# Optimization experiments

Measured on AMD Instinct MI355X. Metric: run time of the kernel, lower is better.

## Reference

```python
import jax, jax.numpy as jnp
import numpy as np

B, N, K = 4, 4096, 16
C_CONT, C_MOT, HID = 64, 64, 128
FEAT = C_CONT + C_MOT


def _conv2d_1x1(W, b, x):
    # x: [B, Cin, N, K] -> [B, Cout, N, K]
    return jnp.einsum('oc,bcnk->bonk', W, x) + b[None, :, None, None]


def _conv1d_1x1(W, b, x):
    # x: [B, Cin, N] -> [B, Cout, N]
    return jnp.einsum('oc,bcn->bon', W, x) + b[None, :, None]


def setup_inputs() -> dict:
    key = jax.random.key(0)
    ks = jax.random.split(key, 13)
    def w(k, shape):
        fan_in = shape[-1]
        return jax.random.normal(k, shape, dtype=jnp.float32) / np.sqrt(fan_in)
    return {
        'H0': jax.random.normal(ks[0], (B, HID, N), dtype=jnp.float32),
        'points0': jax.random.normal(ks[1], (B, 3, N), dtype=jnp.float32),
        'points1': jax.random.normal(ks[2], (B, 3, N), dtype=jnp.float32),
        'contents1': jax.random.normal(ks[3], (B, C_CONT, N), dtype=jnp.float32),
        'motions1': jax.random.normal(ks[4], (B, C_MOT, N), dtype=jnp.float32),
        'W_R': w(ks[5], (HID, HID + FEAT + 4)),
        'b_R': jnp.zeros((HID,), dtype=jnp.float32),
        'W_Z': w(ks[6], (HID, HID + FEAT + 4)),
        'b_Z': jnp.zeros((HID,), dtype=jnp.float32),
        'W_H0': w(ks[7], (HID, HID + 4)),
        'b_H0': jnp.zeros((HID,), dtype=jnp.float32),
        'W_H1': w(ks[8], (HID, HID + FEAT)),
        'b_H1': jnp.zeros((HID,), dtype=jnp.float32),
    }


def reference(H0, points0, points1, contents1, motions1,
              W_R, b_R, W_Z, b_Z, W_H0, b_H0, W_H1, b_H1):
    p1 = points1.transpose(0, 2, 1)  # [B,N,3] anchors (current frame)
    p0 = points0.transpose(0, 2, 1)  # [B,N,3] queries (last frame)
    # pairwise squared distances [B,N,N]
    sq = (jnp.sum(p1 * p1, -1)[:, :, None]
          + jnp.sum(p0 * p0, -1)[:, None, :]
          - 2.0 * jnp.einsum('bmd,bnd->bmn', p1, p0))
    _, nn_idx = jax.lax.top_k(-sq, K)  # [B,N,K] k-nearest in points0
    # gather neighbor coords and hidden states
    nn_pts = jax.vmap(lambda p, i: p[i])(p0, nn_idx)        # [B,N,K,3]
    nn_H0 = jax.vmap(lambda h, i: h[:, i])(H0, nn_idx)      # [B,C,N,K]
    rela = nn_pts - p1[:, :, None, :]                       # [B,N,K,3]
    dist = jnp.linalg.norm(rela, axis=-1, keepdims=True)    # [B,N,K,1]
    nn_group = jnp.concatenate([rela, dist], -1).transpose(0, 3, 1, 2)  # [B,4,N,K]

    feats = jnp.concatenate([contents1, motions1], axis=1)  # [B,F,N]
    feats_e = jnp.broadcast_to(feats[..., None], feats.shape + (K,))  # [B,F,N,K]

    x_rz = jnp.concatenate([nn_group, nn_H0, feats_e], axis=1)  # [B,4+C+F,N,K]
    gate_R = jax.nn.sigmoid(jnp.max(_conv2d_1x1(W_R, b_R, x_rz), axis=-1))  # [B,C,N]
    gate_Z = jax.nn.sigmoid(jnp.max(_conv2d_1x1(W_Z, b_Z, x_rz), axis=-1))  # [B,C,N]

    x_h = jnp.concatenate([nn_group, nn_H0], axis=1)  # [B,4+C,N,K]
    H1_0 = jnp.max(_conv2d_1x1(W_H0, b_H0, x_h), axis=-1)  # [B,C,N]

    H1_1 = jnp.tanh(_conv1d_1x1(W_H1, b_H1,
                                jnp.concatenate([feats, gate_R * H1_0], axis=1)))
    return gate_Z * H1_0 + (1.0 - gate_Z) * H1_1
```

## Files before the change

### kernel.cpp

```cpp
#include <hip/hip_runtime.h>
#include <math.h>


#define BIGV 1e30f

typedef __attribute__((ext_vector_type(8))) short bf16x8;
typedef __attribute__((ext_vector_type(16))) float f32x16;

#define MFMA32(a, b, c) __builtin_amdgcn_mfma_f32_32x32x16_bf16(a, b, c, 0, 0, 0)

__device__ __forceinline__ unsigned short f2bf(float x) {
  unsigned int u = __float_as_uint(x);
  unsigned int r = u + 0x7fffu + ((u >> 16) & 1u);
  return (unsigned short)(r >> 16);
}

__global__ __launch_bounds__(256) void k_transpose(const float* __restrict__ H0,
                                                   unsigned short* __restrict__ H0tb) {
  __shared__ float tile[16][17];
  int blk = blockIdx.x;
  int b = blk >> 11;
  int rem = blk & 2047;
  int c0 = (rem >> 8) << 4;
  int n0 = (rem & 255) << 4;
  int tr = threadIdx.x >> 4, tc = threadIdx.x & 15;
  tile[tr][tc] = H0[((b << 7) + c0 + tr) * 4096 + n0 + tc];
  __syncthreads();
  H0tb[((b << 12) + n0 + tr) * 128 + c0 + tc] = f2bf(tile[tc][tr]);
}

__global__ __launch_bounds__(256) void k_pack(const float* __restrict__ p0,
                                              float4* __restrict__ P0p) {
  int t = blockIdx.x * 256 + threadIdx.x;
  int b = t >> 12, j = t & 4095;
  const float* P0 = p0 + b * 3 * 4096;
  float x = P0[j], y = P0[4096 + j], z = P0[8192 + j];
  P0p[t] = make_float4(x, y, z, x * x + y * y + z * z);
}

__device__ __forceinline__ unsigned long long knn_key(float v, int j) {
  unsigned int u = __float_as_uint(v);
  unsigned int mask = (unsigned int)(((int)u) >> 31) | 0x80000000u;
  return ((unsigned long long)(u ^ mask) << 32) | (unsigned int)j;
}

__global__ __launch_bounds__(256) void k_knn(const float4* __restrict__ P0p,
                                             const float* __restrict__ p1,
                                             int* __restrict__ nn) {
  const int wv = threadIdx.x >> 6, lane = threadIdx.x & 63;
  const int g = (blockIdx.x << 2) + wv;
  const int b = g >> 12, m = g & 4095;
  const float* P1 = p1 + b * 3 * 4096;
  const float x1 = P1[m], y1 = P1[4096 + m], z1 = P1[8192 + m];
  const float s1 = x1 * x1 + y1 * y1 + z1 * z1;
  const float nx = -2.0f * x1, ny = -2.0f * y1, nz = -2.0f * z1;
  const float4* C = P0p + (b << 12);

  float v0 = BIGV, v1 = BIGV, v2 = BIGV, v3 = BIGV;
  int j0 = 0, j1 = 0, j2 = 0, j3 = 0;
#pragma unroll 8
  for (int t = 0; t < 64; ++t) {
    const int j = (t << 6) + lane;
    float4 c = C[j];
    float sq = fmaf(nz, c.z, fmaf(ny, c.y, fmaf(nx, c.x, s1 + c.w)));
    bool c0_ = sq < v0, c1_ = sq < v1, c2_ = sq < v2, c3_ = sq < v3;
    j3 = c3_ ? (c2_ ? j2 : j) : j3;
    j2 = c2_ ? (c1_ ? j1 : j) : j2;
    j1 = c1_ ? (c0_ ? j0 : j) : j1;
    j0 = c0_ ? j : j0;
    v3 = __builtin_amdgcn_fmed3f(sq, v2, v3);
    v2 = __builtin_amdgcn_fmed3f(sq, v1, v2);
    v1 = __builtin_amdgcn_fmed3f(sq, v0, v1);
    v0 = fminf(sq, v0);
  }

  const unsigned long long INFK = ~0ull;
  unsigned long long k0 = knn_key(v0, j0), k1 = knn_key(v1, j1);
  unsigned long long k2 = knn_key(v2, j2), k3 = knn_key(v3, j3);

  unsigned long long wkey = 0;
  unsigned long long lastk = 0;
#pragma unroll 1
  for (int r = 0; r < 16; ++r) {
    unsigned long long mk;
    if (!__any((int)(k0 == INFK))) {
      mk = k0;
    } else {
      mk = k0;
      if (k0 == INFK) {
#pragma unroll 1
        for (int t = 0; t < 64; ++t) {
          const int j = (t << 6) + lane;
          float4 c = C[j];
          float sq = fmaf(nz, c.z, fmaf(ny, c.y, fmaf(nx, c.x, s1 + c.w)));
          unsigned long long kk = knn_key(sq, j);
          if (kk > lastk && kk < mk) mk = kk;
        }
      }
    }
#pragma unroll
    for (int off = 1; off < 64; off <<= 1) {
      unsigned long long ok = __shfl_xor(mk, off);
      mk = (ok < mk) ? ok : mk;
    }
    if (lane == r) wkey = mk;
    lastk = mk;
    if (k0 == mk) { k0 = k1; k1 = k2; k2 = k3; k3 = INFK; }
  }
  const int ob = ((b << 12) + m) << 4;
  if (lane < 16) nn[ob + lane] = (int)(unsigned int)wkey;
}

__global__ __launch_bounds__(256) void k_prep(const float* __restrict__ W_R,
                                              const float* __restrict__ W_Z,
                                              const float* __restrict__ W_H0,
                                              const float* __restrict__ W_H1,
                                              unsigned short* __restrict__ WmainP,
                                              unsigned short* __restrict__ WfeP) {
  int t = blockIdx.x * 256 + threadIdx.x;
  if (t < 6912) {
    int l = t & 63;
    int f = t >> 6;
    int ks = f % 9, T = f / 9;
    int col = T * 32 + (l & 31);
    int kb = ks * 16 + ((l >> 5) << 3);
    const float* W; int stride, row;
    if (col < 128)      { W = W_R;  stride = 260; row = col; }
    else if (col < 256) { W = W_Z;  stride = 260; row = col - 128; }
    else                { W = W_H0; stride = 132; row = col - 256; }
    unsigned int u[4];
#pragma unroll
    for (int i2 = 0; i2 < 4; ++i2) {
      float a0, a1;
      int k0 = kb + 2 * i2, k1 = k0 + 1;
      a0 = (k0 < 128) ? W[row * stride + 4 + k0] : ((k0 < 132) ? W[row * stride + (k0 - 128)] : 0.f);
      a1 = (k1 < 128) ? W[row * stride + 4 + k1] : ((k1 < 132) ? W[row * stride + (k1 - 128)] : 0.f);
      u[i2] = (unsigned int)f2bf(a0) | ((unsigned int)f2bf(a1) << 16);
    }
    uint4 pk; pk.x = u[0]; pk.y = u[1]; pk.z = u[2]; pk.w = u[3];
    *(uint4*)&WmainP[t * 8] = pk;
  } else if (t < 13056) {
    int idx = t - 6912;
    int l = idx & 63;
    int ks = (idx >> 6) & 7;
    int tid = idx >> 9;
    int kb = ks * 16 + ((l >> 5) << 3);
    unsigned int u[4];
#pragma unroll
    for (int i2 = 0; i2 < 4; ++i2) {
      int k0 = kb + 2 * i2, k1 = k0 + 1;
      float a0, a1;
      if (tid < 8) {
        int col = tid * 32 + (l & 31);
        const float* W = (col < 128) ? W_R : W_Z;
        int row = (col < 128) ? col : col - 128;
        a0 = W[row * 260 + 132 + k0];
        a1 = W[row * 260 + 132 + k1];
      } else {
        int row = (tid - 8) * 32 + (l & 31);
        a0 = W_H1[row * 256 + k0];
        a1 = W_H1[row * 256 + k1];
      }
      u[i2] = (unsigned int)f2bf(a0) | ((unsigned int)f2bf(a1) << 16);
    }
    uint4 pk; pk.x = u[0]; pk.y = u[1]; pk.z = u[2]; pk.w = u[3];
    *(uint4*)&WfeP[idx * 8] = pk;
  }
}

__global__ __launch_bounds__(256, 2) void k_mainmax(
    const unsigned short* __restrict__ H0tb, const int* __restrict__ nn,
    const float* __restrict__ p0, const float* __restrict__ p1,
    const float* __restrict__ ct, const float* __restrict__ mo,
    const short* __restrict__ WmainP, const short* __restrict__ WfeP,
    float* __restrict__ SmG) {
  __shared__ unsigned short Xb[2][18][32][8];
  __shared__ unsigned short FeL[16][32][8];

  const int t = threadIdx.x;
  const int g = blockIdx.x;
  const int b = g >> 7;
  const int n0 = (g & 127) << 5;
  const int w = t >> 6, lane = t & 63;
  const int l31 = lane & 31, h = lane >> 5;

  bf16x8 wfm[3][9];
#pragma unroll
  for (int tt = 0; tt < 3; ++tt)
#pragma unroll
    for (int ks = 0; ks < 9; ++ks)
      wfm[tt][ks] = *(const bf16x8*)&WmainP[(((3 * w + tt) * 9 + ks) * 64 + lane) * 8];

  auto stageX = [&](int buf, int pi) {
    int s = t >> 3, c = t & 7;
    int n = n0 + pi + ((s >> 4) << 4);
    int j = nn[(((b << 12) + n) << 4) + (s & 15)];
    const uint4* src = (const uint4*)&H0tb[((b << 12) + j) * 128];
    *(uint4*)&Xb[buf][c][s][0]     = src[c];
    *(uint4*)&Xb[buf][c + 8][s][0] = src[c + 8];
    if (t < 32) {
      int s2 = t;
      int n2 = n0 + pi + ((s2 >> 4) << 4);
      int j2 = nn[(((b << 12) + n2) << 4) + (s2 & 15)];
      const float* P1b = p1 + b * 3 * 4096;
      const float* P0b = p0 + b * 3 * 4096;
      float rx = P0b[j2] - P1b[n2];
      float ry = P0b[4096 + j2] - P1b[4096 + n2];
      float rz = P0b[8192 + j2] - P1b[8192 + n2];
      float dd = sqrtf(rx * rx + ry * ry + rz * rz);
      uint4 pk;
      pk.x = (unsigned int)f2bf(rx) | ((unsigned int)f2bf(ry) << 16);
      pk.y = (unsigned int)f2bf(rz) | ((unsigned int)f2bf(dd) << 16);
      pk.z = 0u; pk.w = 0u;
      *(uint4*)&Xb[buf][16][s2][0] = pk;
      uint4 z; z.x = 0u; z.y = 0u; z.z = 0u; z.w = 0u;
      *(uint4*)&Xb[buf][17][s2][0] = z;
    }
  };

  {
    int s = t >> 3, kg = t & 7;
    int n = n0 + s;
#pragma unroll
    for (int half = 0; half < 2; ++half) {
      int kgg = kg + 8 * half;
      const float* src = half ? (mo + b * 64 * 4096) : (ct + b * 64 * 4096);
      int ch = kg * 8;
      unsigned int u[4];
#pragma unroll
      for (int i2 = 0; i2 < 4; ++i2) {
        float a0 = src[(ch + 2 * i2) * 4096 + n];
        float a1 = src[(ch + 2 * i2 + 1) * 4096 + n];
        u[i2] = (unsigned int)f2bf(a0) | ((unsigned int)f2bf(a1) << 16);
      }
      uint4 pk; pk.x = u[0]; pk.y = u[1]; pk.z = u[2]; pk.w = u[3];
      *(uint4*)&FeL[kgg][s][0] = pk;
    }
  }
  stageX(0, 0);
  __syncthreads();

  float accF[3][16];
#pragma unroll
  for (int tt = 0; tt < 3; ++tt)
#pragma unroll
    for (int r = 0; r < 16; ++r) accF[tt][r] = 0.f;

  bf16x8 fe[8];
#pragma unroll
  for (int ks = 0; ks < 8; ++ks) fe[ks] = *(const bf16x8*)&FeL[2 * ks + h][l31][0];

#pragma unroll
  for (int tt = 0; tt < 3; ++tt) {
    if (3 * w + tt < 8) {
      f32x16 a;
#pragma unroll
      for (int r = 0; r < 16; ++r) a[r] = 0.f;
#pragma unroll
      for (int ks = 0; ks < 8; ++ks) {
        bf16x8 wf = *(const bf16x8*)&WfeP[(((3 * w + tt) * 8 + ks) * 64 + lane) * 8];
        a = MFMA32(fe[ks], wf, a);
      }
#pragma unroll
      for (int r = 0; r < 16; ++r) accF[tt][r] = a[r];
    }
  }

#pragma unroll
  for (int pi = 0; pi < 16; ++pi) {
    if (pi < 15) stageX((pi + 1) & 1, pi + 1);

    f32x16 a0, a1, a2;
#pragma unroll
    for (int r = 0; r < 16; ++r) { a0[r] = 0.f; a1[r] = 0.f; a2[r] = 0.f; }
#pragma unroll
    for (int ks = 0; ks < 9; ++ks) {
      bf16x8 xf = *(const bf16x8*)&Xb[pi & 1][2 * ks + h][l31][0];
      a0 = MFMA32(xf, wfm[0][ks], a0);
      a1 = MFMA32(xf, wfm[1][ks], a1);
      a2 = MFMA32(xf, wfm[2][ks], a2);
    }

    const int ra = (pi & 3) + (((pi >> 3) & 1) << 2);
    const int ha = (pi >> 2) & 1;
    const bool sel = (h == ha);
#pragma unroll
    for (int tt = 0; tt < 3; ++tt) {
      const f32x16& a = (tt == 0) ? a0 : ((tt == 1) ? a1 : a2);
      float ma = fmaxf(fmaxf(fmaxf(a[0], a[1]), fmaxf(a[2], a[3])),
                       fmaxf(fmaxf(a[4], a[5]), fmaxf(a[6], a[7])));
      float mb = fmaxf(fmaxf(fmaxf(a[8], a[9]), fmaxf(a[10], a[11])),
                       fmaxf(fmaxf(a[12], a[13]), fmaxf(a[14], a[15])));
      ma = fmaxf(ma, __shfl_xor(ma, 32));
      mb = fmaxf(mb, __shfl_xor(mb, 32));
      accF[tt][ra]     += sel ? ma : 0.f;
      accF[tt][ra + 8] += sel ? mb : 0.f;
    }
    __syncthreads();
  }

  const long base = (long)(g << 5) * 512;
#pragma unroll
  for (int tt = 0; tt < 3; ++tt)
#pragma unroll
    for (int r = 0; r < 16; ++r) {
      int pt = (r & 3) + ((r >> 2) << 3) + 4 * h;
      SmG[base + (long)pt * 512 + 96 * w + 32 * tt + l31] = accF[tt][r];
    }

  {
    f32x16 a;
#pragma unroll
    for (int r = 0; r < 16; ++r) a[r] = 0.f;
#pragma unroll
    for (int ks = 0; ks < 8; ++ks) {
      bf16x8 feq = *(const bf16x8*)&FeL[2 * ks + h][l31][0];
      bf16x8 wf = *(const bf16x8*)&WfeP[(((8 + w) * 8 + ks) * 64 + lane) * 8];
      a = MFMA32(feq, wf, a);
    }
#pragma unroll
    for (int r = 0; r < 16; ++r) {
      int pt = (r & 3) + ((r >> 2) << 3) + 4 * h;
      SmG[base + (long)pt * 512 + 384 + 32 * w + l31] = a[r];
    }
  }
}

__global__ __launch_bounds__(512) void k_epi(
    const float* __restrict__ SmG, const float* __restrict__ W_H1,
    const float* __restrict__ b_R, const float* __restrict__ b_Z,
    const float* __restrict__ b_H0, const float* __restrict__ b_H1,
    float* __restrict__ out) {
  extern __shared__ float sm[];
  float* Wl = sm;
  float* Pr = sm + 128 * 132;
  const int t = threadIdx.x;
  const int blk = blockIdx.x;
  const long gp0 = (long)blk * 64;
  const int b = (int)(gp0 >> 12);
  const int nb = (int)(gp0 & 4095);

#pragma unroll
  for (int i = 0; i < 8; ++i) {
    int idx = i * 512 + t;
    int row = idx >> 5, c4 = (idx & 31) << 2;
    float4 v = *(const float4*)&W_H1[row * 256 + 128 + c4];
    *(float4*)&Wl[row * 132 + c4] = v;
  }
  {
    int pt = t >> 3, cb = (t & 7) << 4;
    const float* row = SmG + (gp0 + pt) * 512;
#pragma unroll
    for (int ii = 0; ii < 4; ++ii) {
      int c = cb + ii * 4;
      float4 Rv = *(const float4*)&row[c];
      float4 Hv = *(const float4*)&row[256 + c];
      float4 br = *(const float4*)&b_R[c];
      float4 bh = *(const float4*)&b_H0[c];
      float4 pv;
      pv.x = (Hv.x + bh.x) / (1.f + __expf(-(Rv.x + br.x)));
      pv.y = (Hv.y + bh.y) / (1.f + __expf(-(Rv.y + br.y)));
      pv.z = (Hv.z + bh.z) / (1.f + __expf(-(Rv.z + br.z)));
      pv.w = (Hv.w + bh.w) / (1.f + __expf(-(Rv.w + br.w)));
      *(float4*)&Pr[pt * 128 + c] = pv;
    }
  }
  __syncthreads();

  const int r = t & 127, pg = t >> 7;
  float acc[16];
#pragma unroll
  for (int p = 0; p < 16; ++p) acc[p] = 0.f;
#pragma unroll 4
  for (int c0 = 0; c0 < 32; ++c0) {
    float4 wv = *(const float4*)&Wl[r * 132 + (c0 << 2)];
#pragma unroll
    for (int p = 0; p < 16; ++p) {
      float4 pv = *(const float4*)&Pr[(pg * 16 + p) * 128 + (c0 << 2)];
      acc[p] = fmaf(wv.x, pv.x, acc[p]);
      acc[p] = fmaf(wv.y, pv.y, acc[p]);
      acc[p] = fmaf(wv.z, pv.z, acc[p]);
      acc[p] = fmaf(wv.w, pv.w, acc[p]);
    }
  }

  const float bZr = b_Z[r], bH0r = b_H0[r], bH1r = b_H1[r];
  float ov[16];
#pragma unroll
  for (int p = 0; p < 16; ++p) {
    const float* prow = SmG + (gp0 + pg * 16 + p) * 512;
    float Z   = prow[128 + r];
    float H0v = prow[256 + r];
    float Aa  = prow[384 + r];
    float gZ = 1.f / (1.f + __expf(-(Z + bZr)));
    float h0 = H0v + bH0r;
    float h1 = tanhf(Aa + acc[p] + bH1r);
    ov[p] = gZ * h0 + (1.f - gZ) * h1;
  }
  long ob = (long)(b * 128 + r) * 4096 + nb + pg * 16;
#pragma unroll
  for (int q = 0; q < 4; ++q) {
    float4 v; v.x = ov[4 * q]; v.y = ov[4 * q + 1]; v.z = ov[4 * q + 2]; v.w = ov[4 * q + 3];
    *(float4*)&out[ob + 4 * q] = v;
  }
}

extern "C" void kernel_launch(void* const* d_in, const int* in_sizes, int n_in,
                              void* d_out, int out_size, void* d_ws, size_t ws_size,
                              hipStream_t stream) {
  const float* H0  = (const float*)d_in[0];
  const float* p0  = (const float*)d_in[1];
  const float* p1  = (const float*)d_in[2];
  const float* ct  = (const float*)d_in[3];
  const float* mo  = (const float*)d_in[4];
  const float* W_R = (const float*)d_in[5];
  const float* b_R = (const float*)d_in[6];
  const float* W_Z = (const float*)d_in[7];
  const float* b_Z = (const float*)d_in[8];
  const float* W_H0 = (const float*)d_in[9];
  const float* b_H0 = (const float*)d_in[10];
  const float* W_H1 = (const float*)d_in[11];
  const float* b_H1 = (const float*)d_in[12];
  float* out = (float*)d_out;

  unsigned short* H0tb   = (unsigned short*)d_ws;
  int* nn                = (int*)((char*)d_ws + 4ull * 1024 * 1024);
  unsigned short* WmainP = (unsigned short*)((char*)d_ws + 5ull * 1024 * 1024);
  unsigned short* WfeP   = (unsigned short*)((char*)d_ws + 5ull * 1024 * 1024 + 512ull * 1024);
  float4* P0p            = (float4*)((char*)d_ws + 6ull * 1024 * 1024);
  float* SmG             = (float*)((char*)d_ws + 8ull * 1024 * 1024);

  k_transpose<<<8192, 256, 0, stream>>>(H0, H0tb);
  k_pack<<<64, 256, 0, stream>>>(p0, P0p);
  k_knn<<<4096, 256, 0, stream>>>(P0p, p1, nn);
  k_prep<<<51, 256, 0, stream>>>(W_R, W_Z, W_H0, W_H1, WmainP, WfeP);
  k_mainmax<<<512, 256, 0, stream>>>(H0tb, nn, p0, p1, ct, mo,
                                     (const short*)WmainP, (const short*)WfeP, SmG);
  const int epi_lds = (128 * 132 + 64 * 128) * 4;
  hipFuncSetAttribute((const void*)k_epi, hipFuncAttributeMaxDynamicSharedMemorySize, epi_lds);
  k_epi<<<256, 512, epi_lds, stream>>>(SmG, W_H1, b_R, b_Z, b_H0, b_H1, out);
}
```

Before: 294.7 us.

## Batch KNN queries per wave, fuse pack into transpose, MFMA epilogue GEMM

Each KNN wave now handles four query points, so every candidate load is reused four times and the number of launches and shuffle reductions per point drops. The P0 packing kernel is merged into a larger-tile H0 transpose kernel, which writes bf16 pairs. The epilogue GEMM over W_H1 moves from scalar FMA to bf16 MFMA, with a hi/lo split of the activations to keep accuracy, and output is staged through LDS for coalesced stores. Costs include higher register pressure in KNN, which has fewer blocks, and a split-precision approximation in the epilogue.

```diff
diff --git a/kernel.cpp b/kernel.cpp
--- a/kernel.cpp
+++ b/kernel.cpp
@@ -14,28 +14,43 @@
   unsigned int r = u + 0x7fffu + ((u >> 16) & 1u);
   return (unsigned short)(r >> 16);
 }
+__device__ __forceinline__ float bf2f(unsigned short u) {
+  return __uint_as_float(((unsigned int)u) << 16);
+}
 
 __global__ __launch_bounds__(256) void k_transpose(const float* __restrict__ H0,
-                                                   unsigned short* __restrict__ H0tb) {
-  __shared__ float tile[16][17];
-  int blk = blockIdx.x;
-  int b = blk >> 11;
-  int rem = blk & 2047;
-  int c0 = (rem >> 8) << 4;
-  int n0 = (rem & 255) << 4;
-  int tr = threadIdx.x >> 4, tc = threadIdx.x & 15;
-  tile[tr][tc] = H0[((b << 7) + c0 + tr) * 4096 + n0 + tc];
+                                                   unsigned short* __restrict__ H0tb,
+                                                   const float* __restrict__ p0,
+                                                   float4* __restrict__ P0p) {
+  const int blk = blockIdx.x;
+  if (blk >= 512) {
+    int t = ((blk - 512) << 8) + threadIdx.x;
+    int b = t >> 12, j = t & 4095;
+    const float* P0 = p0 + b * 3 * 4096;
+    float x = P0[j], y = P0[4096 + j], z = P0[8192 + j];
+    P0p[t] = make_float4(x, y, z, x * x + y * y + z * z);
+    return;
+  }
+  __shared__ float tile[64][65];
+  const int b = blk >> 7;
+  const int rem = blk & 127;
+  const int c0 = (rem >> 6) << 6;
+  const int n0 = (rem & 63) << 6;
+#pragma unroll
+  for (int it = 0; it < 16; ++it) {
+    int idx = (it << 8) + threadIdx.x;
+    int r = idx >> 6, cl = idx & 63;
+    tile[r][cl] = H0[((b << 7) + c0 + r) * 4096 + n0 + cl];
+  }
   __syncthreads();
-  H0tb[((b << 12) + n0 + tr) * 128 + c0 + tc] = f2bf(tile[tc][tr]);
-}
-
-__global__ __launch_bounds__(256) void k_pack(const float* __restrict__ p0,
-                                              float4* __restrict__ P0p) {
-  int t = blockIdx.x * 256 + threadIdx.x;
-  int b = t >> 12, j = t & 4095;
-  const float* P0 = p0 + b * 3 * 4096;
-  float x = P0[j], y = P0[4096 + j], z = P0[8192 + j];
-  P0p[t] = make_float4(x, y, z, x * x + y * y + z * z);
+#pragma unroll
+  for (int it = 0; it < 8; ++it) {
+    int idx = (it << 8) + threadIdx.x;
+    int nr = idx >> 5, cc2 = (idx & 31) << 1;
+    unsigned int v = (unsigned int)f2bf(tile[cc2][nr]) |
+                     ((unsigned int)f2bf(tile[cc2 + 1][nr]) << 16);
+    *(unsigned int*)&H0tb[((b << 12) + n0 + nr) * 128 + c0 + cc2] = v;
+  }
 }
 
 __device__ __forceinline__ unsigned long long knn_key(float v, int j) {
@@ -48,67 +63,96 @@
                                              const float* __restrict__ p1,
                                              int* __restrict__ nn) {
   const int wv = threadIdx.x >> 6, lane = threadIdx.x & 63;
-  const int g = (blockIdx.x << 2) + wv;
-  const int b = g >> 12, m = g & 4095;
+  const int g0 = ((blockIdx.x << 2) + wv) << 2;
+  const int b = g0 >> 12, m0 = g0 & 4095;
   const float* P1 = p1 + b * 3 * 4096;
-  const float x1 = P1[m], y1 = P1[4096 + m], z1 = P1[8192 + m];
-  const float s1 = x1 * x1 + y1 * y1 + z1 * z1;
-  const float nx = -2.0f * x1, ny = -2.0f * y1, nz = -2.0f * z1;
+  float nx[4], ny[4], nz[4], s1[4];
+#pragma unroll
+  for (int q = 0; q < 4; ++q) {
+    float x1 = P1[m0 + q], y1 = P1[4096 + m0 + q], z1 = P1[8192 + m0 + q];
+    s1[q] = x1 * x1 + y1 * y1 + z1 * z1;
+    nx[q] = -2.f * x1; ny[q] = -2.f * y1; nz[q] = -2.f * z1;
+  }
   const float4* C = P0p + (b << 12);
 
-  float v0 = BIGV, v1 = BIGV, v2 = BIGV, v3 = BIGV;
-  int j0 = 0, j1 = 0, j2 = 0, j3 = 0;
-#pragma unroll 8
-  for (int t = 0; t < 64; ++t) {
-    const int j = (t << 6) + lane;
+  float v0[4], v1[4], v2[4], v3[4];
+  int j0[4], j1[4], j2[4], j3[4];
+#pragma unroll
+  for (int q = 0; q < 4; ++q) {
+    v0[q] = v1[q] = v2[q] = v3[q] = BIGV;
+    j0[q] = j1[q] = j2[q] = j3[q] = 0;
+  }
+#pragma unroll 4
+  for (int tt = 0; tt < 64; ++tt) {
+    const int j = (tt << 6) + lane;
     float4 c = C[j];
-    float sq = fmaf(nz, c.z, fmaf(ny, c.y, fmaf(nx, c.x, s1 + c.w)));
-    bool c0_ = sq < v0, c1_ = sq < v1, c2_ = sq < v2, c3_ = sq < v3;
-    j3 = c3_ ? (c2_ ? j2 : j) : j3;
-    j2 = c2_ ? (c1_ ? j1 : j) : j2;
-    j1 = c1_ ? (c0_ ? j0 : j) : j1;
-    j0 = c0_ ? j : j0;
-    v3 = __builtin_amdgcn_fmed3f(sq, v2, v3);
-    v2 = __builtin_amdgcn_fmed3f(sq, v1, v2);
-    v1 = __builtin_amdgcn_fmed3f(sq, v0, v1);
-    v0 = fminf(sq, v0);
+#pragma unroll
+    for (int q = 0; q < 4; ++q) {
+      float sq = fmaf(nz[q], c.z, fmaf(ny[q], c.y, fmaf(nx[q], c.x, s1[q] + c.w)));
+      bool c0_ = sq < v0[q], c1_ = sq < v1[q], c2_ = sq < v2[q], c3_ = sq < v3[q];
+      j3[q] = c3_ ? (c2_ ? j2[q] : j) : j3[q];
+      j2[q] = c2_ ? (c1_ ? j1[q] : j) : j2[q];
+      j1[q] = c1_ ? (c0_ ? j0[q] : j) : j1[q];
+      j0[q] = c0_ ? j : j0[q];
+      v3[q] = __builtin_amdgcn_fmed3f(sq, v2[q], v3[q]);
+      v2[q] = __builtin_amdgcn_fmed3f(sq, v1[q], v2[q]);
+      v1[q] = __builtin_amdgcn_fmed3f(sq, v0[q], v1[q]);
+      v0[q] = fminf(sq, v0[q]);
+    }
   }
 
   const unsigned long long INFK = ~0ull;
-  unsigned long long k0 = knn_key(v0, j0), k1 = knn_key(v1, j1);
-  unsigned long long k2 = knn_key(v2, j2), k3 = knn_key(v3, j3);
-
-  unsigned long long wkey = 0;
-  unsigned long long lastk = 0;
+  unsigned long long k0[4], k1[4], k2[4], k3[4], wkey[4], lastk[4];
+#pragma unroll
+  for (int q = 0; q < 4; ++q) {
+    k0[q] = knn_key(v0[q], j0[q]); k1[q] = knn_key(v1[q], j1[q]);
+    k2[q] = knn_key(v2[q], j2[q]); k3[q] = knn_key(v3[q], j3[q]);
+    wkey[q] = 0; lastk[q] = 0;
+  }
 #pragma unroll 1
   for (int r = 0; r < 16; ++r) {
-    unsigned long long mk;
-    if (!__any((int)(k0 == INFK))) {
-      mk = k0;
-    } else {
-      mk = k0;
-      if (k0 == INFK) {
+    unsigned long long mk[4];
+#pragma unroll
+    for (int q = 0; q < 4; ++q) {
+      mk[q] = k0[q];
+      if (__any((int)(k0[q] == INFK))) {
+        if (k0[q] == INFK) {
+          float x1 = P1[m0 + q], y1 = P1[4096 + m0 + q], z1 = P1[8192 + m0 + q];
+          float s1q = x1 * x1 + y1 * y1 + z1 * z1;
+          float nxq = -2.f * x1, nyq = -2.f * y1, nzq = -2.f * z1;
+          unsigned long long best = INFK;
 #pragma unroll 1
-        for (int t = 0; t < 64; ++t) {
-          const int j = (t << 6) + lane;
-          float4 c = C[j];
-          float sq = fmaf(nz, c.z, fmaf(ny, c.y, fmaf(nx, c.x, s1 + c.w)));
-          unsigned long long kk = knn_key(sq, j);
-          if (kk > lastk && kk < mk) mk = kk;
+          for (int t2 = 0; t2 < 64; ++t2) {
+            const int j = (t2 << 6) + lane;
+            float4 c = C[j];
+            float sq = fmaf(nzq, c.z, fmaf(nyq, c.y, fmaf(nxq, c.x, s1q + c.w)));
+            unsigned long long kk = knn_key(sq, j);
+            if (kk > lastk[q] && kk < best) best = kk;
+          }
+          mk[q] = best;
         }
       }
     }
 #pragma unroll
     for (int off = 1; off < 64; off <<= 1) {
-      unsigned long long ok = __shfl_xor(mk, off);
-      mk = (ok < mk) ? ok : mk;
-    }
-    if (lane == r) wkey = mk;
-    lastk = mk;
-    if (k0 == mk) { k0 = k1; k1 = k2; k2 = k3; k3 = INFK; }
-  }
-  const int ob = ((b << 12) + m) << 4;
-  if (lane < 16) nn[ob + lane] = (int)(unsigned int)wkey;
+#pragma unroll
+      for (int q = 0; q < 4; ++q) {
+        unsigned long long ok = __shfl_xor(mk[q], off);
+        mk[q] = (ok < mk[q]) ? ok : mk[q];
+      }
+    }
+#pragma unroll
+    for (int q = 0; q < 4; ++q) {
+      if (lane == r) wkey[q] = mk[q];
+      lastk[q] = mk[q];
+      if (k0[q] == mk[q]) { k0[q] = k1[q]; k1[q] = k2[q]; k2[q] = k3[q]; k3[q] = INFK; }
+    }
+  }
+  if (lane < 16) {
+#pragma unroll
+    for (int q = 0; q < 4; ++q)
+      nn[(((b << 12) + m0 + q) << 4) + lane] = (int)(unsigned int)wkey[q];
+  }
 }
 
 __global__ __launch_bounds__(256) void k_prep(const float* __restrict__ W_R,
@@ -116,7 +160,8 @@
                                               const float* __restrict__ W_H0,
                                               const float* __restrict__ W_H1,
                                               unsigned short* __restrict__ WmainP,
-                                              unsigned short* __restrict__ WfeP) {
+                                              unsigned short* __restrict__ WfeP,
+                                              unsigned short* __restrict__ WprP) {
   int t = blockIdx.x * 256 + threadIdx.x;
   if (t < 6912) {
     int l = t & 63;
@@ -165,6 +210,23 @@
     }
     uint4 pk; pk.x = u[0]; pk.y = u[1]; pk.z = u[2]; pk.w = u[3];
     *(uint4*)&WfeP[idx * 8] = pk;
+  } else if (t < 15104) {
+    int idx = t - 13056;
+    int l = idx & 63;
+    int ks = (idx >> 6) & 7;
+    int T = idx >> 9;
+    int row = T * 32 + (l & 31);
+    int kb = ks * 16 + ((l >> 5) << 3);
+    unsigned int u[4];
+#pragma unroll
+    for (int i2 = 0; i2 < 4; ++i2) {
+      int k0 = kb + 2 * i2;
+      float a0 = W_H1[row * 256 + 128 + k0];
+      float a1 = W_H1[row * 256 + 128 + k0 + 1];
+      u[i2] = (unsigned int)f2bf(a0) | ((unsigned int)f2bf(a1) << 16);
+    }
+    uint4 pk; pk.x = u[0]; pk.y = u[1]; pk.z = u[2]; pk.w = u[3];
+    *(uint4*)&WprP[idx * 8] = pk;
   }
 }
 
@@ -326,82 +388,103 @@
   }
 }
 
-__global__ __launch_bounds__(512) void k_epi(
-    const float* __restrict__ SmG, const float* __restrict__ W_H1,
+__device__ __forceinline__ int prh_idx(int hl, int pt, int c) {
+  int blkc = (c >> 3) ^ (pt & 15);
+  return hl * 8192 + pt * 128 + blkc * 8 + (c & 7);
+}
+
+__global__ __launch_bounds__(256) void k_epi2(
+    const float* __restrict__ SmG, const short* __restrict__ WprP,
     const float* __restrict__ b_R, const float* __restrict__ b_Z,
     const float* __restrict__ b_H0, const float* __restrict__ b_H1,
     float* __restrict__ out) {
-  extern __shared__ float sm[];
-  float* Wl = sm;
-  float* Pr = sm + 128 * 132;
+  __shared__ __align__(16) float lds[64 * 132];
+  unsigned short* PrH = (unsigned short*)lds;
   const int t = threadIdx.x;
   const int blk = blockIdx.x;
   const long gp0 = (long)blk * 64;
   const int b = (int)(gp0 >> 12);
   const int nb = (int)(gp0 & 4095);
-
-#pragma unroll
-  for (int i = 0; i < 8; ++i) {
-    int idx = i * 512 + t;
-    int row = idx >> 5, c4 = (idx & 31) << 2;
-    float4 v = *(const float4*)&W_H1[row * 256 + 128 + c4];
-    *(float4*)&Wl[row * 132 + c4] = v;
-  }
+  const int w = t >> 6, lane = t & 63, l31 = lane & 31, h = lane >> 5;
+
   {
-    int pt = t >> 3, cb = (t & 7) << 4;
+    const int pt = t >> 2, cg = (t & 3) << 5;
     const float* row = SmG + (gp0 + pt) * 512;
 #pragma unroll
-    for (int ii = 0; ii < 4; ++ii) {
-      int c = cb + ii * 4;
+    for (int i = 0; i < 8; ++i) {
+      int c = cg + (i << 2);
       float4 Rv = *(const float4*)&row[c];
       float4 Hv = *(const float4*)&row[256 + c];
       float4 br = *(const float4*)&b_R[c];
       float4 bh = *(const float4*)&b_H0[c];
-      float4 pv;
-      pv.x = (Hv.x + bh.x) / (1.f + __expf(-(Rv.x + br.x)));
-      pv.y = (Hv.y + bh.y) / (1.f + __expf(-(Rv.y + br.y)));
-      pv.z = (Hv.z + bh.z) / (1.f + __expf(-(Rv.z + br.z)));
-      pv.w = (Hv.w + bh.w) / (1.f + __expf(-(Rv.w + br.w)));
-      *(float4*)&Pr[pt * 128 + c] = pv;
+      float pr0 = (Hv.x + bh.x) / (1.f + __expf(-(Rv.x + br.x)));
+      float pr1 = (Hv.y + bh.y) / (1.f + __expf(-(Rv.y + br.y)));
+      float pr2 = (Hv.z + bh.z) / (1.f + __expf(-(Rv.z + br.z)));
+      float pr3 = (Hv.w + bh.w) / (1.f + __expf(-(Rv.w + br.w)));
+      unsigned short h0s = f2bf(pr0), h1s = f2bf(pr1), h2s = f2bf(pr2), h3s = f2bf(pr3);
+      unsigned short l0s = f2bf(pr0 - bf2f(h0s)), l1s = f2bf(pr1 - bf2f(h1s));
+      unsigned short l2s = f2bf(pr2 - bf2f(h2s)), l3s = f2bf(pr3 - bf2f(h3s));
+      *(uint2*)&PrH[prh_idx(0, pt, c)] =
+          make_uint2((unsigned int)h0s | ((unsigned int)h1s << 16),
+                     (unsigned int)h2s | ((unsigned int)h3s << 16));
+      *(uint2*)&PrH[prh_idx(1, pt, c)] =
+          make_uint2((unsigned int)l0s | ((unsigned int)l1s << 16),
+                     (unsigned int)l2s | ((unsigned int)l3s << 16));
     }
   }
   __syncthreads();
 
-  const int r = t & 127, pg = t >> 7;
-  float acc[16];
-#pragma unroll
-  for (int p = 0; p < 16; ++p) acc[p] = 0.f;
-#pragma unroll 4
-  for (int c0 = 0; c0 < 32; ++c0) {
-    float4 wv = *(const float4*)&Wl[r * 132 + (c0 << 2)];
-#pragma unroll
-    for (int p = 0; p < 16; ++p) {
-      float4 pv = *(const float4*)&Pr[(pg * 16 + p) * 128 + (c0 << 2)];
-      acc[p] = fmaf(wv.x, pv.x, acc[p]);
-      acc[p] = fmaf(wv.y, pv.y, acc[p]);
-      acc[p] = fmaf(wv.z, pv.z, acc[p]);
-      acc[p] = fmaf(wv.w, pv.w, acc[p]);
-    }
-  }
-
-  const float bZr = b_Z[r], bH0r = b_H0[r], bH1r = b_H1[r];
-  float ov[16];
-#pragma unroll
-  for (int p = 0; p < 16; ++p) {
-    const float* prow = SmG + (gp0 + pg * 16 + p) * 512;
-    float Z   = prow[128 + r];
-    float H0v = prow[256 + r];
-    float Aa  = prow[384 + r];
-    float gZ = 1.f / (1.f + __expf(-(Z + bZr)));
-    float h0 = H0v + bH0r;
-    float h1 = tanhf(Aa + acc[p] + bH1r);
-    ov[p] = gZ * h0 + (1.f - gZ) * h1;
-  }
-  long ob = (long)(b * 128 + r) * 4096 + nb + pg * 16;
-#pragma unroll
-  for (int q = 0; q < 4; ++q) {
-    float4 v; v.x = ov[4 * q]; v.y = ov[4 * q + 1]; v.z = ov[4 * q + 2]; v.w = ov[4 * q + 3];
-    *(float4*)&out[ob + 4 * q] = v;
+  f32x16 ac0, ac1;
+#pragma unroll
+  for (int r = 0; r < 16; ++r) { ac0[r] = 0.f; ac1[r] = 0.f; }
+#pragma unroll
+  for (int ks = 0; ks < 8; ++ks) {
+    bf16x8 wf = *(const bf16x8*)&WprP[((w * 8 + ks) * 64 + lane) * 8];
+    int cb = ks * 16 + (h << 3);
+    bf16x8 a0h = *(const bf16x8*)&PrH[prh_idx(0, l31, cb)];
+    bf16x8 a0l = *(const bf16x8*)&PrH[prh_idx(1, l31, cb)];
+    bf16x8 a1h = *(const bf16x8*)&PrH[prh_idx(0, 32 + l31, cb)];
+    bf16x8 a1l = *(const bf16x8*)&PrH[prh_idx(1, 32 + l31, cb)];
+    ac0 = MFMA32(a0h, wf, ac0);
+    ac0 = MFMA32(a0l, wf, ac0);
+    ac1 = MFMA32(a1h, wf, ac1);
+    ac1 = MFMA32(a1l, wf, ac1);
+  }
+  __syncthreads();
+
+  float* Ot = lds;
+  const int rglob = (w << 5) + l31;
+  const float bZr = b_Z[rglob], bH0r = b_H0[rglob], bH1r = b_H1[rglob];
+#pragma unroll
+  for (int pt_t = 0; pt_t < 2; ++pt_t) {
+#pragma unroll
+    for (int r = 0; r < 16; ++r) {
+      float hBv = pt_t ? ac1[r] : ac0[r];
+      int pt = (pt_t << 5) + (r & 3) + ((r >> 2) << 3) + (h << 2);
+      const float* prow = SmG + (gp0 + pt) * 512;
+      float Z   = prow[128 + rglob];
+      float H0v = prow[256 + rglob];
+      float Aa  = prow[384 + rglob];
+      float gZ = 1.f / (1.f + __expf(-(Z + bZr)));
+      float h0 = H0v + bH0r;
+      float h1 = tanhf(Aa + hBv + bH1r);
+      Ot[pt * 132 + rglob] = gZ * h0 + (1.f - gZ) * h1;
+    }
+  }
+  __syncthreads();
+
+  {
+    const int rr = t >> 1, half = t & 1;
+#pragma unroll
+    for (int qq = 0; qq < 8; ++qq) {
+      int pb = (half << 5) + (qq << 2);
+      float4 v;
+      v.x = Ot[(pb + 0) * 132 + rr];
+      v.y = Ot[(pb + 1) * 132 + rr];
+      v.z = Ot[(pb + 2) * 132 + rr];
+      v.w = Ot[(pb + 3) * 132 + rr];
+      *(float4*)&out[(long)((b << 7) + rr) * 4096 + nb + pb] = v;
+    }
   }
 }
 
@@ -427,16 +510,14 @@
   int* nn                = (int*)((char*)d_ws + 4ull * 1024 * 1024);
   unsigned short* WmainP = (unsigned short*)((char*)d_ws + 5ull * 1024 * 1024);
   unsigned short* WfeP   = (unsigned short*)((char*)d_ws + 5ull * 1024 * 1024 + 512ull * 1024);
+  unsigned short* WprP   = (unsigned short*)((char*)d_ws + 5ull * 1024 * 1024 + 768ull * 1024);
   float4* P0p            = (float4*)((char*)d_ws + 6ull * 1024 * 1024);
   float* SmG             = (float*)((char*)d_ws + 8ull * 1024 * 1024);
 
-  k_transpose<<<8192, 256, 0, stream>>>(H0, H0tb);
-  k_pack<<<64, 256, 0, stream>>>(p0, P0p);
-  k_knn<<<4096, 256, 0, stream>>>(P0p, p1, nn);
-  k_prep<<<51, 256, 0, stream>>>(W_R, W_Z, W_H0, W_H1, WmainP, WfeP);
+  k_transpose<<<576, 256, 0, stream>>>(H0, H0tb, p0, P0p);
+  k_knn<<<1024, 256, 0, stream>>>(P0p, p1, nn);
+  k_prep<<<59, 256, 0, stream>>>(W_R, W_Z, W_H0, W_H1, WmainP, WfeP, WprP);
   k_mainmax<<<512, 256, 0, stream>>>(H0tb, nn, p0, p1, ct, mo,
                                      (const short*)WmainP, (const short*)WfeP, SmG);
-  const int epi_lds = (128 * 132 + 64 * 128) * 4;
-  hipFuncSetAttribute((const void*)k_epi, hipFuncAttributeMaxDynamicSharedMemorySize, epi_lds);
-  k_epi<<<256, 512, epi_lds, stream>>>(SmG, W_H1, b_R, b_Z, b_H0, b_H1, out);
-}
+  k_epi2<<<256, 256, 0, stream>>>(SmG, (const short*)WprP, b_R, b_Z, b_H0, b_H1, out);
+}
```

New measurement: 368.5 us. 25.0% more time.
